# Kernel tuning notes

Measured on AMD Instinct MI355X. Metric: run time of the kernel, lower is better.

## Reference

```python
import jax, jax.numpy as jnp
import numpy as np

# Dimensions
B, C, H, W = 16, 256, 32, 32
CO, DK, DV, NH = 256, 128, 128, 8   # channels_out, depth_k, depth_v, num_heads
KS = 3                              # conv kernel size
DKH, DVH = DK // NH, DV // NH


def setup_inputs() -> dict:
    key = jax.random.key(0)
    ks = jax.random.split(key, 4)
    s = 0.05
    return {
        "x": jax.random.normal(ks[0], (B, C, H, W), jnp.float32),
        # conv branch: 3x3 conv -> channels_out - depth_v = 128, HWIO layout
        "conv_w": jax.random.normal(ks[1], (KS, KS, C, CO - DV), jnp.float32) * s,
        "conv_b": jnp.zeros((CO - DV,), jnp.float32),
        # 1x1 QKV conv: 2*depth_k + depth_v output channels
        "qkv_w": jax.random.normal(ks[2], (2 * DK + DV, C), jnp.float32) * s,
        "qkv_b": jnp.zeros((2 * DK + DV,), jnp.float32),
        # 1x1 output projection conv: depth_v -> depth_v
        "proj_w": jax.random.normal(ks[3], (DV, DV), jnp.float32) * s,
        "proj_b": jnp.zeros((DV,), jnp.float32),
    }


def reference(x, conv_w, conv_b, qkv_w, qkv_b, proj_w, proj_b):
    # --- conv branch (3x3, SAME padding, NCHW) ---
    conv_out = jax.lax.conv_general_dilated(
        x, conv_w, window_strides=(1, 1), padding='SAME',
        dimension_numbers=('NCHW', 'HWIO', 'NCHW'))
    conv_out = conv_out + conv_b[None, :, None, None]

    # --- attention branch ---
    # 1x1 conv == channel matmul
    kqv = jnp.einsum('bchw,oc->bohw', x, qkv_w) + qkv_b[None, :, None, None]
    # tf.split order: k, q, v
    k, q, v = jnp.split(kqv, [DK, 2 * DK], axis=1)
    q = q * (DKH ** -0.5)

    def heads(t, d):  # (B, NH*d, H, W) -> (B, NH, H*W, d)
        return t.reshape(B, NH, d, H * W).transpose(0, 1, 3, 2)

    qh, kh, vh = heads(q, DKH), heads(k, DKH), heads(v, DVH)
    logits = jnp.einsum('bnqd,bnkd->bnqk', qh, kh)          # (B,NH,HW,HW)
    weights = jax.nn.softmax(logits, axis=-1)
    attn = jnp.einsum('bnqk,bnkd->bnqd', weights, vh)       # (B,NH,HW,DVH)
    # combine heads, head-major channel order -> (B, DV, H, W)
    attn = attn.transpose(0, 1, 3, 2).reshape(B, DV, H, W)
    attn_out = jnp.einsum('bchw,oc->bohw', attn, proj_w) + proj_b[None, :, None, None]

    return jnp.concatenate([conv_out, attn_out], axis=1)
```

## Files before the change

### kernel.cpp

```cpp
#include <hip/hip_runtime.h>
#include <hip/hip_bf16.h>


#define Bn   16
#define Cin  256
#define HWp  1024
#define COn  256
#define NHn  8

typedef short short8  __attribute__((ext_vector_type(8)));
typedef short short4v __attribute__((ext_vector_type(4)));
typedef float f32x4   __attribute__((ext_vector_type(4)));
typedef float f32x16  __attribute__((ext_vector_type(16)));

__device__ inline short bf16_rne(float f) {
  unsigned u = __builtin_bit_cast(unsigned, f);
  u += 0x7fffu + ((u >> 16) & 1u);
  return (short)(u >> 16);
}

__device__ inline unsigned pkbf(float a, float b) {
  __hip_bfloat162 h = __float22bfloat162_rn(make_float2(a, b));
  unsigned u;
  __builtin_memcpy(&u, &h, 4);
  return u;
}

__device__ inline void store_bf8(short* dst, const float* f) {
  uint4 u;
  u.x = pkbf(f[0], f[1]); u.y = pkbf(f[2], f[3]);
  u.z = pkbf(f[4], f[5]); u.w = pkbf(f[6], f[7]);
  *(uint4*)dst = u;
}

__global__ __launch_bounds__(256) void prep_all(
    const float* __restrict__ cw, const float* __restrict__ qw,
    const float* __restrict__ pw, short* __restrict__ wfc,
    short* __restrict__ wfq, short* __restrict__ wfp)
{
  const int gid  = blockIdx.x * 256 + threadIdx.x;
  const int lane = gid & 63, frag = gid >> 6;
  const int l15 = lane & 15, q = lane >> 4;
  short8 pk;
  if (frag < 576) {
    const int cf = frag & 7, cq = (frag >> 3) & 7, kk = frag >> 6;
    const int co = cf * 16 + l15, c = cq * 32 + q * 8;
#pragma unroll
    for (int j = 0; j < 8; ++j)
      pk[j] = bf16_rne(cw[(size_t)(kk * Cin + c + j) * 128 + co]);
    *(short8*)(wfc + (size_t)frag * 512 + lane * 8) = pk;
  } else if (frag < 768) {
    const int f = frag - 576;
    const int rt = f >> 3, kf = f & 7;
    const int o = rt * 16 + l15, c = kf * 32 + q * 8;
#pragma unroll
    for (int j = 0; j < 8; ++j) pk[j] = bf16_rne(qw[o * Cin + c + j]);
    *(short8*)(wfq + (size_t)f * 512 + lane * 8) = pk;
  } else if (frag < 800) {
    const int f = frag - 768;
    const int rt = f >> 2, kf = f & 3;
    const int o = rt * 16 + l15, c = kf * 32 + q * 8;
#pragma unroll
    for (int j = 0; j < 8; ++j) pk[j] = bf16_rne(pw[o * 128 + c + j]);
    *(short8*)(wfp + (size_t)f * 512 + lane * 8) = pk;
  }
}

__global__ __launch_bounds__(256) void prep_x(
    const float* __restrict__ x, short* __restrict__ xt)
{
  __shared__ short t[32][262];
  const int tid = threadIdx.x;
  const int hw0 = (blockIdx.x & 3) * 256;
  const int c0  = ((blockIdx.x >> 2) & 7) * 32;
  const int b   = blockIdx.x >> 5;

#pragma unroll 4
  for (int cc = 0; cc < 32; ++cc)
    t[cc][tid] = bf16_rne(x[(size_t)(b * Cin + c0 + cc) * HWp + hw0 + tid]);
  __syncthreads();

  for (int s = tid; s < 1024; s += 256) {
    const int hwl = s >> 2, q4 = s & 3;
    short8 pk;
#pragma unroll
    for (int j = 0; j < 8; ++j) pk[j] = t[q4 * 8 + j][hwl];
    *(short8*)&xt[((size_t)(b * HWp + hw0 + hwl)) * 256 + c0 + q4 * 8] = pk;
  }
}

__global__ __launch_bounds__(512) void conv_mfma(
    const short* __restrict__ xt, const short* __restrict__ wf,
    const float* __restrict__ bias, float* __restrict__ out)
{
  __shared__ short xl[2][5712];
  const int tid  = threadIdx.x;
  const int lane = tid & 63, wv = tid >> 6;
  const int l15  = lane & 15, g = lane >> 4;
  const int b  = blockIdx.x >> 4;
  const int h0 = (blockIdx.x & 15) * 2;

  f32x4 acc[4] = {};

#define STAGE(chunk)                                                          \
  {                                                                           \
    const int c0_ = (chunk) * 32;                                             \
    short* dst_ = xl[(chunk) & 1];                                            \
    for (int s = tid; s < 544; s += 512) {                                    \
      const int cell = s >> 2, qq = s & 3;                                    \
      const int r = cell / 34, col = cell - r * 34;                           \
      const int h_in = h0 - 1 + r, w_in = col - 1;                            \
      short8 v = {};                                                          \
      if (h_in >= 0 && h_in < 32 && w_in >= 0 && w_in < 32)                   \
        v = *(const short8*)&xt[((size_t)(b * HWp + h_in * 32 + w_in)) * 256  \
                                + c0_ + qq * 8];                              \
      *(short8*)&dst_[cell * 42 + qq * 8] = v;                                \
    }                                                                         \
  }

  STAGE(0);
  __syncthreads();

  for (int cq = 0; cq < 8; ++cq) {
    if (cq < 7) STAGE(cq + 1);
    const short* cur = xl[cq & 1];
#pragma unroll
    for (int kk = 0; kk < 9; ++kk) {
      const int kh = kk / 3, kw = kk - kh * 3;
      const short8 a0 = *(const short8*)(wf + (size_t)((kk * 8 + cq) * 8 + wv) * 512 + lane * 8);
#pragma unroll
      for (int bf = 0; bf < 4; ++bf) {
        const int m = bf * 16 + l15;
        const int r = (m >> 5) + kh, col = (m & 31) + kw;
        const short8 xv = *(const short8*)&cur[(r * 34 + col) * 42 + g * 8];
        acc[bf] = __builtin_amdgcn_mfma_f32_16x16x32_bf16(a0, xv, acc[bf], 0, 0, 0);
      }
    }
    __syncthreads();
  }
#undef STAGE

  const int cob = wv * 16 + g * 4;
#pragma unroll
  for (int r = 0; r < 4; ++r) {
    const int co = cob + r;
    const float bv = bias[co];
    float* op = out + (size_t)(b * COn + co) * HWp + h0 * 32 + l15;
#pragma unroll
    for (int bf = 0; bf < 4; ++bf)
      op[bf * 16] = acc[bf][r] + bv;
  }
}

__global__ __launch_bounds__(512) void qkv_mfma(
    const short* __restrict__ xt, const short* __restrict__ wfq,
    const float* __restrict__ bias, short* __restrict__ qbuf,
    short* __restrict__ kbuf, short* __restrict__ vtbuf)
{
  __shared__ short xl[16384];
  const int tid = threadIdx.x, lane = tid & 63, wv = tid >> 6;
  const int l15 = lane & 15, g = lane >> 4;
  const int hw0 = blockIdx.x * 64;
  const int b   = blockIdx.y;

  {
    const int qq = tid & 3, kf = (tid >> 2) & 7, hl = tid >> 5;
#pragma unroll
    for (int mt = 0; mt < 4; ++mt) {
      const int p  = ((mt * 8 + kf) * 4 + qq) * 16 + hl;
      const int sw = p ^ ((p >> 4) & 7);
      const short8 v = *(const short8*)&xt[((size_t)(b * HWp + hw0 + mt * 16 + hl)) * 256
                                           + kf * 32 + qq * 8];
      *(short8*)&xl[sw * 8] = v;
    }
  }
  __syncthreads();

  f32x4 acc[3][4] = {};
  for (int kf = 0; kf < 8; ++kf) {
    short8 bfr[4];
#pragma unroll
    for (int mt = 0; mt < 4; ++mt) {
      const int q  = ((mt * 8 + kf) * 4 + g) * 16 + l15;
      const int sw = q ^ ((q >> 4) & 7);
      bfr[mt] = *(const short8*)&xl[sw * 8];
    }
#pragma unroll
    for (int i = 0; i < 3; ++i) {
      const int rt = wv * 3 + i;
      const short8 af = *(const short8*)(wfq + ((size_t)(rt * 8 + kf) * 64 + lane) * 8);
#pragma unroll
      for (int mt = 0; mt < 4; ++mt)
        acc[i][mt] = __builtin_amdgcn_mfma_f32_16x16x32_bf16(af, bfr[mt], acc[i][mt], 0, 0, 0);
    }
  }

#pragma unroll
  for (int i = 0; i < 3; ++i) {
    const int rt = wv * 3 + i;
    float bv[4];
#pragma unroll
    for (int r = 0; r < 4; ++r) bv[r] = bias[rt * 16 + 4 * g + r];
    if (rt < 8) {
      short* kp = kbuf + ((size_t)(b * NHn + rt) * HWp + hw0) * 16 + 4 * g;
#pragma unroll
      for (int mt = 0; mt < 4; ++mt) {
        short4v s;
#pragma unroll
        for (int r = 0; r < 4; ++r) s[r] = bf16_rne(acc[i][mt][r] + bv[r]);
        *(short4v*)(kp + (size_t)(mt * 16 + l15) * 16) = s;
      }
    } else if (rt < 16) {
      short* qp = qbuf + ((size_t)(b * NHn + rt - 8) * HWp + hw0) * 16 + 4 * g;
#pragma unroll
      for (int mt = 0; mt < 4; ++mt) {
        short4v s;
#pragma unroll
        for (int r = 0; r < 4; ++r) s[r] = bf16_rne((acc[i][mt][r] + bv[r]) * 0.25f);
        *(short4v*)(qp + (size_t)(mt * 16 + l15) * 16) = s;
      }
    } else {
      short* vp = vtbuf + (size_t)(b * NHn + rt - 16) * 16 * HWp;
#pragma unroll
      for (int mt = 0; mt < 4; ++mt)
#pragma unroll
        for (int r = 0; r < 4; ++r)
          vp[(size_t)(4 * g + r) * HWp + hw0 + mt * 16 + l15] =
              bf16_rne(acc[i][mt][r] + bv[r]);
    }
  }
}

__global__ __launch_bounds__(256) void attn_mfma(
    const short* __restrict__ qb, const short* __restrict__ kb,
    const short* __restrict__ vt, float* __restrict__ abuf)
{
  __shared__ short P[4][2][32][40];
  const int tid = threadIdx.x, lane = tid & 63, wv = tid >> 6;
  const int l15 = lane & 15, g = lane >> 4;
  const int l31 = lane & 31, hi = lane >> 5;
  const int h = blockIdx.y, b = blockIdx.z, bh = b * NHn + h;
  const int q0 = blockIdx.x * 128 + wv * 32;

  const short* qp = qb + (size_t)bh * HWp * 16;
  const short* kp = kb + (size_t)bh * HWp * 16;
  const short* vp = vt + (size_t)bh * 16 * HWp;

  const short8 qf = *(const short8*)(qp + (size_t)(q0 + l31) * 16 + hi * 8);

  f32x4 o0 = {}, o1 = {};
  float lsum = 0.f;

  for (int kt = 0; kt < HWp; kt += 64) {
#pragma unroll
    for (int t = 0; t < 2; ++t) {
      const int k0 = kt + t * 32;
      const short8 kf = *(const short8*)(kp + (size_t)(k0 + l31) * 16 + hi * 8);
      f32x16 z = {};
      const f32x16 s = __builtin_amdgcn_mfma_f32_32x32x16_bf16(kf, qf, z, 0, 0, 0);
      float p[16];
#pragma unroll
      for (int r = 0; r < 16; ++r) { p[r] = __expf(s[r]); lsum += p[r]; }
#pragma unroll
      for (int rg = 0; rg < 4; ++rg) {
        uint2 u;
        u.x = pkbf(p[4 * rg + 0], p[4 * rg + 1]);
        u.y = pkbf(p[4 * rg + 2], p[4 * rg + 3]);
        *(uint2*)&P[wv][t][l31][8 * rg + 4 * hi] = u;
      }
      const short8 vf = *(const short8*)(vp + (size_t)l15 * HWp + k0 + g * 8);
      const short8 pf0 = *(const short8*)&P[wv][t][l15][g * 8];
      o0 = __builtin_amdgcn_mfma_f32_16x16x32_bf16(vf, pf0, o0, 0, 0, 0);
      const short8 pf1 = *(const short8*)&P[wv][t][16 + l15][g * 8];
      o1 = __builtin_amdgcn_mfma_f32_16x16x32_bf16(vf, pf1, o1, 0, 0, 0);
    }
  }

  const float l  = lsum + __shfl_xor(lsum, 32);
  const float li0 = 1.f / __shfl(l, l15);
  const float li1 = 1.f / __shfl(l, 16 + l15);
#pragma unroll
  for (int r = 0; r < 4; ++r) {
    const int d = 4 * g + r;
    float* op = abuf + (size_t)(b * 128 + h * 16 + d) * HWp + q0;
    op[l15]      = o0[r] * li0;
    op[16 + l15] = o1[r] * li1;
  }
}

__global__ __launch_bounds__(256) void proj_mfma(
    const float* __restrict__ a, const short* __restrict__ wfp,
    const float* __restrict__ bias, float* __restrict__ out)
{
  __shared__ short xl[8192];
  const int tid = threadIdx.x, lane = tid & 63, wv = tid >> 6;
  const int l15 = lane & 15, g = lane >> 4;
  const int hw0 = blockIdx.x * 64;
  const int b   = blockIdx.y;

#pragma unroll
  for (int it = 0; it < 4; ++it) {
    const int p  = it * 256 + tid;
    const int mt = p >> 8, kf = (p >> 6) & 3, qq = (p >> 4) & 3, hl = p & 15;
    const float* ap = a + (size_t)(b * 128 + kf * 32 + qq * 8) * HWp
                        + hw0 + mt * 16 + hl;
    float fv[8];
#pragma unroll
    for (int j = 0; j < 8; ++j) fv[j] = ap[(size_t)j * HWp];
    store_bf8(&xl[p * 8], fv);
  }
  __syncthreads();

  f32x4 acc[2][4] = {};
  for (int kf = 0; kf < 4; ++kf) {
    short8 bfr[4];
#pragma unroll
    for (int mt = 0; mt < 4; ++mt)
      bfr[mt] = *(const short8*)&xl[(((mt * 4 + kf) * 4 + g) * 16 + l15) * 8];
#pragma unroll
    for (int i = 0; i < 2; ++i) {
      const int rt = wv * 2 + i;
      const short8 af = *(const short8*)(wfp + ((size_t)(rt * 4 + kf) * 64 + lane) * 8);
#pragma unroll
      for (int mt = 0; mt < 4; ++mt)
        acc[i][mt] = __builtin_amdgcn_mfma_f32_16x16x32_bf16(af, bfr[mt], acc[i][mt], 0, 0, 0);
    }
  }

#pragma unroll
  for (int i = 0; i < 2; ++i) {
    const int rt = wv * 2 + i;
#pragma unroll
    for (int r = 0; r < 4; ++r) {
      const int o = rt * 16 + 4 * g + r;
      const float bv = bias[o];
      float* op = out + (size_t)(b * COn + 128 + o) * HWp + hw0 + l15;
#pragma unroll
      for (int mt = 0; mt < 4; ++mt)
        op[mt * 16] = acc[i][mt][r] + bv;
    }
  }
}

extern "C" void kernel_launch(void* const* d_in, const int* in_sizes, int n_in,
                              void* d_out, int out_size, void* d_ws, size_t ws_size,
                              hipStream_t stream) {
  const float* x      = (const float*)d_in[0];
  const float* conv_w = (const float*)d_in[1];
  const float* conv_b = (const float*)d_in[2];
  const float* qkv_w  = (const float*)d_in[3];
  const float* qkv_b  = (const float*)d_in[4];
  const float* proj_w = (const float*)d_in[5];
  const float* proj_b = (const float*)d_in[6];
  float* out = (float*)d_out;

  char* wsb = (char*)d_ws;
  short* wfc    = (short*)wsb;
  short* wfq    = (short*)(wsb + (1u << 20));
  short* wfp    = (short*)(wsb + (2u << 20));
  short* qbuf16 = (short*)(wsb + (8u << 20));
  short* kbuf16 = (short*)(wsb + (12u << 20));
  short* vtbuf  = (short*)(wsb + (16u << 20));
  float* abuf   = (float*)(wsb + (20u << 20));
  short* xtbuf  = (short*)(wsb + (28u << 20));

  prep_all  <<<dim3(200), 256, 0, stream>>>(conv_w, qkv_w, proj_w, wfc, wfq, wfp);
  prep_x    <<<dim3(512), 256, 0, stream>>>(x, xtbuf);
  conv_mfma <<<dim3(256), 512, 0, stream>>>(xtbuf, wfc, conv_b, out);
  qkv_mfma  <<<dim3(16, 16), 512, 0, stream>>>(xtbuf, wfq, qkv_b, qbuf16, kbuf16, vtbuf);
  attn_mfma <<<dim3(8, 8, 16), 256, 0, stream>>>(qbuf16, kbuf16, vtbuf, abuf);
  proj_mfma <<<dim3(16, 16), 256, 0, stream>>>(abuf, wfp, proj_b, out);
}
```

Baseline: 182.5 us.

## Fuse prep kernels, pre-pad input, and pass bf16 pixel-major attention output

After: 187.1 us. 2.5% more time.

```diff
diff --git a/kernel.cpp b/kernel.cpp
--- a/kernel.cpp
+++ b/kernel.cpp
@@ -7,6 +7,8 @@
 #define HWp  1024
 #define COn  256
 #define NHn  8
+#define PADW 34
+#define PADA 1156
 
 typedef short short8  __attribute__((ext_vector_type(8)));
 typedef short short4v __attribute__((ext_vector_type(4)));
@@ -26,124 +28,110 @@
   return u;
 }
 
-__device__ inline void store_bf8(short* dst, const float* f) {
-  uint4 u;
-  u.x = pkbf(f[0], f[1]); u.y = pkbf(f[2], f[3]);
-  u.z = pkbf(f[4], f[5]); u.w = pkbf(f[6], f[7]);
-  *(uint4*)dst = u;
-}
-
-__global__ __launch_bounds__(256) void prep_all(
+__global__ __launch_bounds__(256) void prep_fused(
     const float* __restrict__ cw, const float* __restrict__ qw,
-    const float* __restrict__ pw, short* __restrict__ wfc,
-    short* __restrict__ wfq, short* __restrict__ wfp)
-{
-  const int gid  = blockIdx.x * 256 + threadIdx.x;
-  const int lane = gid & 63, frag = gid >> 6;
-  const int l15 = lane & 15, q = lane >> 4;
-  short8 pk;
-  if (frag < 576) {
-    const int cf = frag & 7, cq = (frag >> 3) & 7, kk = frag >> 6;
-    const int co = cf * 16 + l15, c = cq * 32 + q * 8;
-#pragma unroll
-    for (int j = 0; j < 8; ++j)
-      pk[j] = bf16_rne(cw[(size_t)(kk * Cin + c + j) * 128 + co]);
-    *(short8*)(wfc + (size_t)frag * 512 + lane * 8) = pk;
-  } else if (frag < 768) {
-    const int f = frag - 576;
-    const int rt = f >> 3, kf = f & 7;
-    const int o = rt * 16 + l15, c = kf * 32 + q * 8;
-#pragma unroll
-    for (int j = 0; j < 8; ++j) pk[j] = bf16_rne(qw[o * Cin + c + j]);
-    *(short8*)(wfq + (size_t)f * 512 + lane * 8) = pk;
-  } else if (frag < 800) {
-    const int f = frag - 768;
-    const int rt = f >> 2, kf = f & 3;
-    const int o = rt * 16 + l15, c = kf * 32 + q * 8;
-#pragma unroll
-    for (int j = 0; j < 8; ++j) pk[j] = bf16_rne(pw[o * 128 + c + j]);
-    *(short8*)(wfp + (size_t)f * 512 + lane * 8) = pk;
-  }
-}
-
-__global__ __launch_bounds__(256) void prep_x(
-    const float* __restrict__ x, short* __restrict__ xt)
+    const float* __restrict__ pw, const float* __restrict__ x,
+    short* __restrict__ wfc, short* __restrict__ wfq,
+    short* __restrict__ wfp, short* __restrict__ xtp)
 {
   __shared__ short t[32][262];
   const int tid = threadIdx.x;
-  const int hw0 = (blockIdx.x & 3) * 256;
-  const int c0  = ((blockIdx.x >> 2) & 7) * 32;
-  const int b   = blockIdx.x >> 5;
-
+  if (blockIdx.x < 200) {
+    const int gid  = blockIdx.x * 256 + tid;
+    const int lane = gid & 63, frag = gid >> 6;
+    const int l15 = lane & 15, q = lane >> 4;
+    short8 pk;
+    if (frag < 576) {
+      const int cf = frag & 7, cq = (frag >> 3) & 7, kk = frag >> 6;
+      const int co = cf * 16 + l15, c = cq * 32 + q * 8;
+#pragma unroll
+      for (int j = 0; j < 8; ++j)
+        pk[j] = bf16_rne(cw[(size_t)(kk * Cin + c + j) * 128 + co]);
+      *(short8*)(wfc + (size_t)frag * 512 + lane * 8) = pk;
+    } else if (frag < 768) {
+      const int f = frag - 576;
+      const int rt = f >> 3, kf = f & 7;
+      const int o = rt * 16 + l15, c = kf * 32 + q * 8;
+#pragma unroll
+      for (int j = 0; j < 8; ++j) pk[j] = bf16_rne(qw[o * Cin + c + j]);
+      *(short8*)(wfq + (size_t)f * 512 + lane * 8) = pk;
+    } else if (frag < 800) {
+      const int f = frag - 768;
+      const int rt = f >> 2, kf = f & 3;
+      const int o = rt * 16 + l15, c = kf * 32 + q * 8;
+#pragma unroll
+      for (int j = 0; j < 8; ++j) pk[j] = bf16_rne(pw[o * 128 + c + j]);
+      *(short8*)(wfp + (size_t)f * 512 + lane * 8) = pk;
+    }
+  } else {
+    const int bid = blockIdx.x - 200;
+    const int hw0 = (bid & 3) * 256;
+    const int c0  = ((bid >> 2) & 7) * 32;
+    const int b   = bid >> 5;
 #pragma unroll 4
-  for (int cc = 0; cc < 32; ++cc)
-    t[cc][tid] = bf16_rne(x[(size_t)(b * Cin + c0 + cc) * HWp + hw0 + tid]);
-  __syncthreads();
-
-  for (int s = tid; s < 1024; s += 256) {
-    const int hwl = s >> 2, q4 = s & 3;
-    short8 pk;
-#pragma unroll
-    for (int j = 0; j < 8; ++j) pk[j] = t[q4 * 8 + j][hwl];
-    *(short8*)&xt[((size_t)(b * HWp + hw0 + hwl)) * 256 + c0 + q4 * 8] = pk;
+    for (int cc = 0; cc < 32; ++cc)
+      t[cc][tid] = bf16_rne(x[(size_t)(b * Cin + c0 + cc) * HWp + hw0 + tid]);
+    if ((bid & 3) == 0) {
+      for (int i = tid; i < 528; i += 256) {
+        const int fi = i >> 2, qq = i & 3;
+        int r, col;
+        if (fi < 34)       { r = 0;           col = fi; }
+        else if (fi < 68)  { r = 33;          col = fi - 34; }
+        else if (fi < 100) { r = fi - 68 + 1; col = 0; }
+        else               { r = fi - 100 + 1; col = 33; }
+        short8 z = {};
+        *(short8*)&xtp[((size_t)(b * PADA + r * PADW + col)) * 256 + c0 + qq * 8] = z;
+      }
+    }
+    __syncthreads();
+    for (int s = tid; s < 1024; s += 256) {
+      const int pl = s >> 2, qq = s & 3;
+      const int p  = hw0 + pl;
+      const int r  = 1 + (p >> 5), col = 1 + (p & 31);
+      short8 pk;
+#pragma unroll
+      for (int j = 0; j < 8; ++j) pk[j] = t[qq * 8 + j][pl];
+      *(short8*)&xtp[((size_t)(b * PADA + r * PADW + col)) * 256 + c0 + qq * 8] = pk;
+    }
   }
 }
 
 __global__ __launch_bounds__(512) void conv_mfma(
-    const short* __restrict__ xt, const short* __restrict__ wf,
+    const short* __restrict__ xtp, const short* __restrict__ wf,
     const float* __restrict__ bias, float* __restrict__ out)
 {
-  __shared__ short xl[2][5712];
   const int tid  = threadIdx.x;
   const int lane = tid & 63, wv = tid >> 6;
   const int l15  = lane & 15, g = lane >> 4;
   const int b  = blockIdx.x >> 4;
   const int h0 = (blockIdx.x & 15) * 2;
 
+  const short* xb = xtp + (size_t)b * PADA * 256;
   f32x4 acc[4] = {};
 
-#define STAGE(chunk)                                                          \
-  {                                                                           \
-    const int c0_ = (chunk) * 32;                                             \
-    short* dst_ = xl[(chunk) & 1];                                            \
-    for (int s = tid; s < 544; s += 512) {                                    \
-      const int cell = s >> 2, qq = s & 3;                                    \
-      const int r = cell / 34, col = cell - r * 34;                           \
-      const int h_in = h0 - 1 + r, w_in = col - 1;                            \
-      short8 v = {};                                                          \
-      if (h_in >= 0 && h_in < 32 && w_in >= 0 && w_in < 32)                   \
-        v = *(const short8*)&xt[((size_t)(b * HWp + h_in * 32 + w_in)) * 256  \
-                                + c0_ + qq * 8];                              \
-      *(short8*)&dst_[cell * 42 + qq * 8] = v;                                \
-    }                                                                         \
-  }
-
-  STAGE(0);
-  __syncthreads();
-
   for (int cq = 0; cq < 8; ++cq) {
-    if (cq < 7) STAGE(cq + 1);
-    const short* cur = xl[cq & 1];
 #pragma unroll
     for (int kk = 0; kk < 9; ++kk) {
       const int kh = kk / 3, kw = kk - kh * 3;
-      const short8 a0 = *(const short8*)(wf + (size_t)((kk * 8 + cq) * 8 + wv) * 512 + lane * 8);
+      const short8 a = *(const short8*)(wf +
+          (size_t)((kk * 8 + cq) * 8 + wv) * 512 + lane * 8);
+      short8 xv[4];
 #pragma unroll
       for (int bf = 0; bf < 4; ++bf) {
-        const int m = bf * 16 + l15;
-        const int r = (m >> 5) + kh, col = (m & 31) + kw;
-        const short8 xv = *(const short8*)&cur[(r * 34 + col) * 42 + g * 8];
-        acc[bf] = __builtin_amdgcn_mfma_f32_16x16x32_bf16(a0, xv, acc[bf], 0, 0, 0);
-      }
-    }
-    __syncthreads();
-  }
-#undef STAGE
-
-  const int cob = wv * 16 + g * 4;
+        const int row = h0 + (bf >> 1) + kh;
+        const int col = (bf & 1) * 16 + l15 + kw;
+        xv[bf] = *(const short8*)&xb[((size_t)(row * PADW + col)) * 256
+                                     + cq * 32 + g * 8];
+      }
+#pragma unroll
+      for (int bf = 0; bf < 4; ++bf)
+        acc[bf] = __builtin_amdgcn_mfma_f32_16x16x32_bf16(a, xv[bf], acc[bf], 0, 0, 0);
+    }
+  }
+
 #pragma unroll
   for (int r = 0; r < 4; ++r) {
-    const int co = cob + r;
+    const int co = wv * 16 + 4 * g + r;
     const float bv = bias[co];
     float* op = out + (size_t)(b * COn + co) * HWp + h0 * 32 + l15;
 #pragma unroll
@@ -153,7 +141,7 @@
 }
 
 __global__ __launch_bounds__(512) void qkv_mfma(
-    const short* __restrict__ xt, const short* __restrict__ wfq,
+    const short* __restrict__ xtp, const short* __restrict__ wfq,
     const float* __restrict__ bias, short* __restrict__ qbuf,
     short* __restrict__ kbuf, short* __restrict__ vtbuf)
 {
@@ -163,21 +151,34 @@
   const int hw0 = blockIdx.x * 64;
   const int b   = blockIdx.y;
 
+  short8 afr[3], anx[3];
+#pragma unroll
+  for (int i = 0; i < 3; ++i)
+    afr[i] = *(const short8*)(wfq + ((size_t)((wv * 3 + i) * 8 + 0) * 64 + lane) * 8);
+
   {
     const int qq = tid & 3, kf = (tid >> 2) & 7, hl = tid >> 5;
 #pragma unroll
     for (int mt = 0; mt < 4; ++mt) {
       const int p  = ((mt * 8 + kf) * 4 + qq) * 16 + hl;
       const int sw = p ^ ((p >> 4) & 7);
-      const short8 v = *(const short8*)&xt[((size_t)(b * HWp + hw0 + mt * 16 + hl)) * 256
-                                           + kf * 32 + qq * 8];
+      const int px = hw0 + mt * 16 + hl;
+      const int r  = 1 + (px >> 5), col = 1 + (px & 31);
+      const short8 v = *(const short8*)&xtp[((size_t)(b * PADA + r * PADW + col)) * 256
+                                            + kf * 32 + qq * 8];
       *(short8*)&xl[sw * 8] = v;
     }
   }
   __syncthreads();
 
   f32x4 acc[3][4] = {};
+#pragma unroll
   for (int kf = 0; kf < 8; ++kf) {
+    if (kf < 7) {
+#pragma unroll
+      for (int i = 0; i < 3; ++i)
+        anx[i] = *(const short8*)(wfq + ((size_t)((wv * 3 + i) * 8 + kf + 1) * 64 + lane) * 8);
+    }
     short8 bfr[4];
 #pragma unroll
     for (int mt = 0; mt < 4; ++mt) {
@@ -186,12 +187,13 @@
       bfr[mt] = *(const short8*)&xl[sw * 8];
     }
 #pragma unroll
-    for (int i = 0; i < 3; ++i) {
-      const int rt = wv * 3 + i;
-      const short8 af = *(const short8*)(wfq + ((size_t)(rt * 8 + kf) * 64 + lane) * 8);
+    for (int i = 0; i < 3; ++i)
 #pragma unroll
       for (int mt = 0; mt < 4; ++mt)
-        acc[i][mt] = __builtin_amdgcn_mfma_f32_16x16x32_bf16(af, bfr[mt], acc[i][mt], 0, 0, 0);
+        acc[i][mt] = __builtin_amdgcn_mfma_f32_16x16x32_bf16(afr[i], bfr[mt], acc[i][mt], 0, 0, 0);
+    if (kf < 7) {
+#pragma unroll
+      for (int i = 0; i < 3; ++i) afr[i] = anx[i];
     }
   }
 
@@ -233,7 +235,7 @@
 
 __global__ __launch_bounds__(256) void attn_mfma(
     const short* __restrict__ qb, const short* __restrict__ kb,
-    const short* __restrict__ vt, float* __restrict__ abuf)
+    const short* __restrict__ vt, short* __restrict__ at)
 {
   __shared__ short P[4][2][32][40];
   const int tid = threadIdx.x, lane = tid & 63, wv = tid >> 6;
@@ -279,17 +281,17 @@
   const float l  = lsum + __shfl_xor(lsum, 32);
   const float li0 = 1.f / __shfl(l, l15);
   const float li1 = 1.f / __shfl(l, 16 + l15);
-#pragma unroll
-  for (int r = 0; r < 4; ++r) {
-    const int d = 4 * g + r;
-    float* op = abuf + (size_t)(b * 128 + h * 16 + d) * HWp + q0;
-    op[l15]      = o0[r] * li0;
-    op[16 + l15] = o1[r] * li1;
-  }
+  uint2 u0, u1;
+  u0.x = pkbf(o0[0] * li0, o0[1] * li0);
+  u0.y = pkbf(o0[2] * li0, o0[3] * li0);
+  u1.x = pkbf(o1[0] * li1, o1[1] * li1);
+  u1.y = pkbf(o1[2] * li1, o1[3] * li1);
+  *(uint2*)&at[(size_t)(b * HWp + q0 + l15) * 128 + h * 16 + 4 * g]      = u0;
+  *(uint2*)&at[(size_t)(b * HWp + q0 + 16 + l15) * 128 + h * 16 + 4 * g] = u1;
 }
 
 __global__ __launch_bounds__(256) void proj_mfma(
-    const float* __restrict__ a, const short* __restrict__ wfp,
+    const short* __restrict__ at, const short* __restrict__ wfp,
     const float* __restrict__ bias, float* __restrict__ out)
 {
   __shared__ short xl[8192];
@@ -301,13 +303,11 @@
 #pragma unroll
   for (int it = 0; it < 4; ++it) {
     const int p  = it * 256 + tid;
-    const int mt = p >> 8, kf = (p >> 6) & 3, qq = (p >> 4) & 3, hl = p & 15;
-    const float* ap = a + (size_t)(b * 128 + kf * 32 + qq * 8) * HWp
-                        + hw0 + mt * 16 + hl;
-    float fv[8];
-#pragma unroll
-    for (int j = 0; j < 8; ++j) fv[j] = ap[(size_t)j * HWp];
-    store_bf8(&xl[p * 8], fv);
+    const int hl = p & 15, qq = (p >> 4) & 3, kf = (p >> 6) & 3, mt = p >> 8;
+    const short8 v = *(const short8*)&at[((size_t)(b * HWp + hw0 + mt * 16 + hl))
+                                         * 128 + kf * 32 + qq * 8];
+    const int sw = p ^ ((p >> 4) & 7);
+    *(short8*)&xl[sw * 8] = v;
   }
   __syncthreads();
 
@@ -315,8 +315,11 @@
   for (int kf = 0; kf < 4; ++kf) {
     short8 bfr[4];
 #pragma unroll
-    for (int mt = 0; mt < 4; ++mt)
-      bfr[mt] = *(const short8*)&xl[(((mt * 4 + kf) * 4 + g) * 16 + l15) * 8];
+    for (int mt = 0; mt < 4; ++mt) {
+      const int q  = ((mt * 4 + kf) * 4 + g) * 16 + l15;
+      const int sw = q ^ ((q >> 4) & 7);
+      bfr[mt] = *(const short8*)&xl[sw * 8];
+    }
 #pragma unroll
     for (int i = 0; i < 2; ++i) {
       const int rt = wv * 2 + i;
@@ -361,13 +364,13 @@
   short* qbuf16 = (short*)(wsb + (8u << 20));
   short* kbuf16 = (short*)(wsb + (12u << 20));
   short* vtbuf  = (short*)(wsb + (16u << 20));
-  float* abuf   = (float*)(wsb + (20u << 20));
-  short* xtbuf  = (short*)(wsb + (28u << 20));
-
-  prep_all  <<<dim3(200), 256, 0, stream>>>(conv_w, qkv_w, proj_w, wfc, wfq, wfp);
-  prep_x    <<<dim3(512), 256, 0, stream>>>(x, xtbuf);
-  conv_mfma <<<dim3(256), 512, 0, stream>>>(xtbuf, wfc, conv_b, out);
-  qkv_mfma  <<<dim3(16, 16), 512, 0, stream>>>(xtbuf, wfq, qkv_b, qbuf16, kbuf16, vtbuf);
-  attn_mfma <<<dim3(8, 8, 16), 256, 0, stream>>>(qbuf16, kbuf16, vtbuf, abuf);
-  proj_mfma <<<dim3(16, 16), 256, 0, stream>>>(abuf, wfp, proj_b, out);
-}
+  short* atbuf  = (short*)(wsb + (20u << 20));
+  short* xtpbuf = (short*)(wsb + (28u << 20));
+
+  prep_fused<<<dim3(712), 256, 0, stream>>>(conv_w, qkv_w, proj_w, x,
+                                            wfc, wfq, wfp, xtpbuf);
+  conv_mfma <<<dim3(256), 512, 0, stream>>>(xtpbuf, wfc, conv_b, out);
+  qkv_mfma  <<<dim3(16, 16), 512, 0, stream>>>(xtpbuf, wfq, qkv_b, qbuf16, kbuf16, vtbuf);
+  attn_mfma <<<dim3(8, 8, 16), 256, 0, stream>>>(qbuf16, kbuf16, vtbuf, atbuf);
+  proj_mfma <<<dim3(16, 16), 256, 0, stream>>>(atbuf, wfp, proj_b, out);
+}
```
